# Optimization experiments

Measured on AMD Instinct MI355X. Metric: run time of the kernel, lower is better.

Reference implementation:

```python
import jax, jax.numpy as jnp
import numpy as np

NE = 50000   # num edges (nodes of the line graph)
NA = 800000  # adjacency pairs in the edge graph (~avg degree 16)
NC = 100000  # triadic candidates
F = 64       # edge_feat_dim
H = 128      # hidden_dim
L = 3        # num_layers


def setup_inputs() -> dict:
    key = jax.random.key(0)
    ks = iter(jax.random.split(key, 32))

    def w(shape, scale=0.05):
        return jax.random.normal(next(ks), shape, dtype=jnp.float32) * scale

    inp = {
        "edge_features": jax.random.normal(next(ks), (NE, F), dtype=jnp.float32),
        "adj_dst": jnp.sort(jax.random.randint(next(ks), (NA,), 0, NE)),
        "adj_src": jax.random.randint(next(ks), (NA,), 0, NE),
        "cand_i": jax.random.randint(next(ks), (NC,), 0, NE),
        "cand_j": jax.random.randint(next(ks), (NC,), 0, NE),
        # edge encoder: Linear(F,H) -> ReLU -> Linear(H,H)
        "enc_W1": w((F, H)), "enc_b1": jnp.zeros((H,), jnp.float32),
        "enc_W2": w((H, H)), "enc_b2": jnp.zeros((H,), jnp.float32),
        # per-layer message_net: Linear(2H,H) -> ReLU -> Linear(H,H)
        "msg_W1": w((L, 2 * H, H)), "msg_b1": jnp.zeros((L, H), jnp.float32),
        "msg_W2": w((L, H, H)), "msg_b2": jnp.zeros((L, H), jnp.float32),
        # per-layer update_net: Linear(2H,H) -> ReLU -> Linear(H,H)
        "upd_W1": w((L, 2 * H, H)), "upd_b1": jnp.zeros((L, H), jnp.float32),
        "upd_W2": w((L, H, H)), "upd_b2": jnp.zeros((L, H), jnp.float32),
        # triadic predictor: Linear(2H,H)->ReLU->Linear(H,H)->ReLU->Linear(H,1)
        "pred_W1": w((2 * H, H)), "pred_b1": jnp.zeros((H,), jnp.float32),
        "pred_W2": w((H, H)), "pred_b2": jnp.zeros((H,), jnp.float32),
        "pred_W3": w((H, 1)), "pred_b3": jnp.zeros((1,), jnp.float32),
    }
    return inp


def _mlp2(x, W1, b1, W2, b2):
    return jnp.maximum(x @ W1 + b1, 0.0) @ W2 + b2


def reference(edge_features, adj_dst, adj_src, cand_i, cand_j,
              enc_W1, enc_b1, enc_W2, enc_b2,
              msg_W1, msg_b1, msg_W2, msg_b2,
              upd_W1, upd_b1, upd_W2, upd_b2,
              pred_W1, pred_b1, pred_W2, pred_b2, pred_W3, pred_b3):
    # encode edge features -> [NE, H]
    e = _mlp2(edge_features, enc_W1, enc_b1, enc_W2, enc_b2)

    # degree of each edge-node in the line graph
    deg = jax.ops.segment_sum(jnp.ones((adj_dst.shape[0],), e.dtype), adj_dst,
                              num_segments=NE)  # [NE]
    inv_deg = 1.0 / jnp.maximum(deg, 1.0)
    isolated = (deg == 0.0)[:, None]

    for l in range(L):
        # per-pair message: message_net(concat(e_i, e_j))
        pair = jnp.concatenate([e[adj_dst], e[adj_src]], axis=-1)  # [NA, 2H]
        msgs = _mlp2(pair, msg_W1[l], msg_b1[l], msg_W2[l], msg_b2[l])  # [NA, H]
        agg = jax.ops.segment_sum(msgs, adj_dst, num_segments=NE) * inv_deg[:, None]
        # edges with no neighbors: message_net(concat(e_i, e_i))
        self_msg = _mlp2(jnp.concatenate([e, e], axis=-1),
                         msg_W1[l], msg_b1[l], msg_W2[l], msg_b2[l])
        message = jnp.where(isolated, self_msg, agg)
        # update: update_net(concat(e_i, message_i)), then outer ReLU
        e = _mlp2(jnp.concatenate([e, message], axis=-1),
                  upd_W1[l], upd_b1[l], upd_W2[l], upd_b2[l])
        e = jnp.maximum(e, 0.0)

    # triadic predictor on parent-edge pairs (dropout inactive at eval)
    comb = jnp.concatenate([e[cand_i], e[cand_j]], axis=-1)  # [NC, 2H]
    h = jnp.maximum(comb @ pred_W1 + pred_b1, 0.0)
    h = jnp.maximum(h @ pred_W2 + pred_b2, 0.0)
    logits = (h @ pred_W3 + pred_b3)[:, 0]  # [NC]
    probs = jax.nn.sigmoid(logits)
    return probs, logits
```

## Files before the change

### kernel.cpp

```cpp
#include <hip/hip_runtime.h>
#include <hip/hip_bf16.h>

#define NE 50000
#define NA 800000
#define NC 100000

typedef _Float16 f16;
typedef f16 half8 __attribute__((ext_vector_type(8)));
typedef f16 f16x2 __attribute__((ext_vector_type(2)));
typedef float f32x4 __attribute__((ext_vector_type(4)));

#define OFF_ENC1 0
#define OFF_ENC2 8192
#define OFF_MSGPQ 24576
#define OFF_UPD1 122880
#define OFF_UPD2 221184
#define OFF_PREDPQ 270336
#define OFF_PREDW2 303104
#define TOTAL_WT 319488

struct WTArgs {
    const float* src[20];
    int K[20];
    int dstOff[20];
    int dstStride[20];
    int cum[21];
};

__global__ void prep_kernel(WTArgs a, const float* __restrict__ x,
                            f16* __restrict__ wt, f16* __restrict__ xb,
                            int* __restrict__ degI) {
    int gid = blockIdx.x * 256 + threadIdx.x;
    if (gid < a.cum[20]) {
        int j = 0;
#pragma unroll
        for (int i = 1; i < 20; ++i) j += (gid >= a.cum[i]) ? 1 : 0;
        int e = gid - a.cum[j];
        int K = a.K[j];
        int k = e % K;
        int n = e / K;
        wt[a.dstOff[j] + n * a.dstStride[j] + k] = (f16)a.src[j][(size_t)k * 128 + n];
        return;
    }
    int g2 = gid - a.cum[20];
    if (g2 < NE * 16) {
        float4 v = ((const float4*)x)[g2];
        f16x2 p = {(f16)v.x, (f16)v.y}, q = {(f16)v.z, (f16)v.w};
        ((f16x2*)xb)[g2 * 2] = p;
        ((f16x2*)xb)[g2 * 2 + 1] = q;
        return;
    }
    int g3 = g2 - NE * 16;
    if (g3 < NE) degI[g3] = 0;
}

__global__ void fuse_w(const float* __restrict__ msg_W2, const float* __restrict__ msg_b2,
                       const float* __restrict__ upd_W1, const float* __restrict__ upd_b1,
                       f16* __restrict__ wt, float* __restrict__ fbias) {
    int gid = blockIdx.x * 256 + threadIdx.x;
    if (gid >= 3 * 128 * 129) return;
    int l = gid / (128 * 129);
    int rem = gid % (128 * 129);
    int n = rem / 129;
    int kk = rem % 129;
    const float* U1b = upd_W1 + (size_t)l * 32768 + 16384;
    if (kk < 128) {
        const float* w2row = msg_W2 + (size_t)l * 16384 + (size_t)kk * 128;
        float s = 0.0f;
        for (int m = 0; m < 128; ++m) s += w2row[m] * U1b[m * 128 + n];
        wt[OFF_UPD1 + l * 32768 + n * 256 + 128 + kk] = (f16)s;
    } else {
        const float* b2 = msg_b2 + l * 128;
        float s = upd_b1[l * 128 + n];
        for (int m = 0; m < 128; ++m) s += b2[m] * U1b[m * 128 + n];
        fbias[l * 128 + n] = s;
    }
}

__global__ void degseg_kernel(const int* __restrict__ adj_dst, int* __restrict__ degI,
                              int* __restrict__ segStart) {
    int i = blockIdx.x * 256 + threadIdx.x;
    if (i < NA) {
        int d = adj_dst[i];
        atomicAdd(&degI[d], 1);
        if (i == 0 || adj_dst[i - 1] != d) segStart[d] = i;
    }
}

__global__ __launch_bounds__(256) void pair_agg(
    const f16* __restrict__ P, const f16* __restrict__ Q,
    const int* __restrict__ adj_src, const int* __restrict__ segStart,
    const int* __restrict__ degI, f16* __restrict__ hbar) {
    int w = __builtin_amdgcn_readfirstlane(blockIdx.x * 4 + (threadIdx.x >> 6));
    if (w >= NE) return;
    int lane = threadIdx.x & 63;
    f16x2 p2 = ((const f16x2*)P)[(size_t)w * 64 + lane];
    float p0 = (float)p2.x, p1 = (float)p2.y;
    float a0, a1;
    int deg = degI[w];
    if (deg == 0) {
        f16x2 q2 = ((const f16x2*)Q)[(size_t)w * 64 + lane];
        a0 = fmaxf(p0 + (float)q2.x, 0.0f);
        a1 = fmaxf(p1 + (float)q2.y, 0.0f);
    } else {
        int s = segStart[w];
        float x0 = 0.0f, x1 = 0.0f, y0 = 0.0f, y1 = 0.0f;
        int j = 0;
        for (; j + 3 < deg; j += 4) {
            int s0 = adj_src[s + j], s1 = adj_src[s + j + 1];
            int s2 = adj_src[s + j + 2], s3 = adj_src[s + j + 3];
            f16x2 qa = ((const f16x2*)Q)[(size_t)s0 * 64 + lane];
            f16x2 qb = ((const f16x2*)Q)[(size_t)s1 * 64 + lane];
            f16x2 qc = ((const f16x2*)Q)[(size_t)s2 * 64 + lane];
            f16x2 qd = ((const f16x2*)Q)[(size_t)s3 * 64 + lane];
            x0 += fmaxf(p0 + (float)qa.x, 0.0f);
            x1 += fmaxf(p1 + (float)qa.y, 0.0f);
            y0 += fmaxf(p0 + (float)qb.x, 0.0f);
            y1 += fmaxf(p1 + (float)qb.y, 0.0f);
            x0 += fmaxf(p0 + (float)qc.x, 0.0f);
            x1 += fmaxf(p1 + (float)qc.y, 0.0f);
            y0 += fmaxf(p0 + (float)qd.x, 0.0f);
            y1 += fmaxf(p1 + (float)qd.y, 0.0f);
        }
        for (; j < deg; ++j) {
            int s0 = adj_src[s + j];
            f16x2 qa = ((const f16x2*)Q)[(size_t)s0 * 64 + lane];
            x0 += fmaxf(p0 + (float)qa.x, 0.0f);
            x1 += fmaxf(p1 + (float)qa.y, 0.0f);
        }
        float sc = 1.0f / (float)deg;
        a0 = (x0 + y0) * sc;
        a1 = (x1 + y1) * sc;
    }
    f16x2 o;
    o.x = (f16)a0;
    o.y = (f16)a1;
    ((f16x2*)hbar)[(size_t)w * 64 + lane] = o;
}

template <int K1, bool RELU_OUT>
__global__ __launch_bounds__(256, 2) void mlp2pq_kernel(
    const f16* __restrict__ in0, const f16* __restrict__ in1,
    const f16* __restrict__ w1t, const float* __restrict__ b1,
    const f16* __restrict__ w2t, const float* __restrict__ b2,
    f16* __restrict__ oute,
    const f16* __restrict__ wpq, const float* __restrict__ bP,
    f16* __restrict__ P, f16* __restrict__ Q, int numRows) {
    constexpr int KC1 = K1 / 32;
    constexpr int SA = K1 + 8;
    constexpr int SH = 136;
    constexpr int ABY = 64 * SA * 2;
    constexpr int HEBY = 64 * SH * 2 * 2;
    constexpr int BYTES = ABY > HEBY ? ABY : HEBY;
    __shared__ __align__(16) char U[BYTES];
    f16* Abuf = (f16*)U;
    f16* Hbuf = (f16*)U;
    f16* Ebuf = (f16*)(U + 64 * SH * 2);

    const int t = threadIdx.x;
    const int lane = t & 63, wave = t >> 6;
    const int quad = lane >> 4, mn = lane & 15;
    const int n0 = wave * 32;
    const int rbase = blockIdx.x << 6;

    constexpr int UPR = K1 / 8;
    constexpr int USH = (K1 == 256) ? 5 : 3;
#pragma unroll
    for (int it = 0; it < (64 * UPR) / 256; ++it) {
        int u = it * 256 + t;
        int row = u >> USH;
        int k = (u & (UPR - 1)) * 8;
        int gr = rbase + row;
        half8 v = {};
        if (gr < numRows) {
            const f16* src;
            if constexpr (K1 == 64)
                src = in0 + (size_t)gr * 64 + k;
            else
                src = (k < 128) ? (in0 + (size_t)gr * 128 + k)
                                : (in1 + (size_t)gr * 128 + (k - 128));
            v = *(const half8*)src;
        }
        *(half8*)(Abuf + row * SA + k) = v;
    }

    {
        half8 w1f[KC1][2];
#pragma unroll
        for (int kc = 0; kc < KC1; ++kc)
#pragma unroll
            for (int nt = 0; nt < 2; ++nt)
                w1f[kc][nt] = *(const half8*)(w1t + (size_t)(n0 + nt * 16 + mn) * K1 + kc * 32 + quad * 8);
        float b1c[2] = {b1[n0 + mn], b1[n0 + 16 + mn]};
        __syncthreads();

        f32x4 acc[4][2];
#pragma unroll
        for (int mt = 0; mt < 4; ++mt) {
            acc[mt][0] = (f32x4){b1c[0], b1c[0], b1c[0], b1c[0]};
            acc[mt][1] = (f32x4){b1c[1], b1c[1], b1c[1], b1c[1]};
        }
#pragma unroll
        for (int kc = 0; kc < KC1; ++kc) {
            half8 af[4];
#pragma unroll
            for (int mt = 0; mt < 4; ++mt)
                af[mt] = *(const half8*)(Abuf + (mt * 16 + mn) * SA + kc * 32 + quad * 8);
#pragma unroll
            for (int mt = 0; mt < 4; ++mt) {
                acc[mt][0] = __builtin_amdgcn_mfma_f32_16x16x32_f16(af[mt], w1f[kc][0], acc[mt][0], 0, 0, 0);
                acc[mt][1] = __builtin_amdgcn_mfma_f32_16x16x32_f16(af[mt], w1f[kc][1], acc[mt][1], 0, 0, 0);
            }
        }
        __syncthreads();
#pragma unroll
        for (int mt = 0; mt < 4; ++mt)
#pragma unroll
            for (int nt = 0; nt < 2; ++nt)
#pragma unroll
                for (int r = 0; r < 4; ++r)
                    Hbuf[(mt * 16 + quad * 4 + r) * SH + n0 + nt * 16 + mn] =
                        (f16)fmaxf(acc[mt][nt][r], 0.0f);
        __syncthreads();
    }

    {
        half8 w2f[4][2];
#pragma unroll
        for (int kc = 0; kc < 4; ++kc)
#pragma unroll
            for (int nt = 0; nt < 2; ++nt)
                w2f[kc][nt] = *(const half8*)(w2t + (size_t)(n0 + nt * 16 + mn) * 128 + kc * 32 + quad * 8);
        float b2c[2] = {b2[n0 + mn], b2[n0 + 16 + mn]};

        f32x4 acc2[4][2];
#pragma unroll
        for (int mt = 0; mt < 4; ++mt) {
            acc2[mt][0] = (f32x4){b2c[0], b2c[0], b2c[0], b2c[0]};
            acc2[mt][1] = (f32x4){b2c[1], b2c[1], b2c[1], b2c[1]};
        }
#pragma unroll
        for (int kc = 0; kc < 4; ++kc) {
            half8 af[4];
#pragma unroll
            for (int mt = 0; mt < 4; ++mt)
                af[mt] = *(const half8*)(Hbuf + (mt * 16 + mn) * SH + kc * 32 + quad * 8);
#pragma unroll
            for (int mt = 0; mt < 4; ++mt) {
                acc2[mt][0] = __builtin_amdgcn_mfma_f32_16x16x32_f16(af[mt], w2f[kc][0], acc2[mt][0], 0, 0, 0);
                acc2[mt][1] = __builtin_amdgcn_mfma_f32_16x16x32_f16(af[mt], w2f[kc][1], acc2[mt][1], 0, 0, 0);
            }
        }
#pragma unroll
        for (int mt = 0; mt < 4; ++mt)
#pragma unroll
            for (int nt = 0; nt < 2; ++nt)
#pragma unroll
                for (int r = 0; r < 4; ++r) {
                    float v = acc2[mt][nt][r];
                    if constexpr (RELU_OUT) v = fmaxf(v, 0.0f);
                    f16 hv = (f16)v;
                    int lr = mt * 16 + quad * 4 + r;
                    Ebuf[lr * SH + n0 + nt * 16 + mn] = hv;
                    int gr = rbase + lr;
                    if (gr < numRows) oute[(size_t)gr * 128 + n0 + nt * 16 + mn] = hv;
                }
        __syncthreads();
    }

    {
        half8 wpa[4][2];
#pragma unroll
        for (int kc = 0; kc < 4; ++kc)
#pragma unroll
            for (int nt = 0; nt < 2; ++nt)
                wpa[kc][nt] = *(const half8*)(wpq + (size_t)(n0 + nt * 16 + mn) * 128 + kc * 32 + quad * 8);
        float bpc[2] = {bP[n0 + mn], bP[n0 + 16 + mn]};
        f32x4 accp[4][2];
#pragma unroll
        for (int mt = 0; mt < 4; ++mt) {
            accp[mt][0] = (f32x4){bpc[0], bpc[0], bpc[0], bpc[0]};
            accp[mt][1] = (f32x4){bpc[1], bpc[1], bpc[1], bpc[1]};
        }
#pragma unroll
        for (int kc = 0; kc < 4; ++kc) {
            half8 af[4];
#pragma unroll
            for (int mt = 0; mt < 4; ++mt)
                af[mt] = *(const half8*)(Ebuf + (mt * 16 + mn) * SH + kc * 32 + quad * 8);
#pragma unroll
            for (int mt = 0; mt < 4; ++mt) {
                accp[mt][0] = __builtin_amdgcn_mfma_f32_16x16x32_f16(af[mt], wpa[kc][0], accp[mt][0], 0, 0, 0);
                accp[mt][1] = __builtin_amdgcn_mfma_f32_16x16x32_f16(af[mt], wpa[kc][1], accp[mt][1], 0, 0, 0);
            }
        }
#pragma unroll
        for (int mt = 0; mt < 4; ++mt)
#pragma unroll
            for (int nt = 0; nt < 2; ++nt)
#pragma unroll
                for (int r = 0; r < 4; ++r) {
                    int gr = rbase + mt * 16 + quad * 4 + r;
                    if (gr < numRows)
                        P[(size_t)gr * 128 + n0 + nt * 16 + mn] = (f16)accp[mt][nt][r];
                }
    }

    {
        half8 wpb[4][2];
#pragma unroll
        for (int kc = 0; kc < 4; ++kc)
#pragma unroll
            for (int nt = 0; nt < 2; ++nt)
                wpb[kc][nt] = *(const half8*)(wpq + 16384 + (size_t)(n0 + nt * 16 + mn) * 128 + kc * 32 + quad * 8);
        f32x4 accq[4][2];
#pragma unroll
        for (int mt = 0; mt < 4; ++mt) {
            accq[mt][0] = (f32x4){0.0f, 0.0f, 0.0f, 0.0f};
            accq[mt][1] = (f32x4){0.0f, 0.0f, 0.0f, 0.0f};
        }
#pragma unroll
        for (int kc = 0; kc < 4; ++kc) {
            half8 af[4];
#pragma unroll
            for (int mt = 0; mt < 4; ++mt)
                af[mt] = *(const half8*)(Ebuf + (mt * 16 + mn) * SH + kc * 32 + quad * 8);
#pragma unroll
            for (int mt = 0; mt < 4; ++mt) {
                accq[mt][0] = __builtin_amdgcn_mfma_f32_16x16x32_f16(af[mt], wpb[kc][0], accq[mt][0], 0, 0, 0);
                accq[mt][1] = __builtin_amdgcn_mfma_f32_16x16x32_f16(af[mt], wpb[kc][1], accq[mt][1], 0, 0, 0);
            }
        }
#pragma unroll
        for (int mt = 0; mt < 4; ++mt)
#pragma unroll
            for (int nt = 0; nt < 2; ++nt)
#pragma unroll
                for (int r = 0; r < 4; ++r) {
                    int gr = rbase + mt * 16 + quad * 4 + r;
                    if (gr < numRows)
                        Q[(size_t)gr * 128 + n0 + nt * 16 + mn] = (f16)accq[mt][nt][r];
                }
    }
}

__global__ __launch_bounds__(256, 2) void pred_tail(
    const f16* __restrict__ Pp, const f16* __restrict__ Qp,
    const int* __restrict__ ci, const int* __restrict__ cj,
    const f16* __restrict__ w2t, const float* __restrict__ b2,
    const float* __restrict__ w3, const float* __restrict__ b3,
    float* __restrict__ outProb, float* __restrict__ outLogit, int numRows) {
    constexpr int SA = 136;
    constexpr int SO = 133;
    constexpr int BYTES = (64 * SO * 4 > 64 * SA * 2) ? 64 * SO * 4 : 64 * SA * 2;
    __shared__ __align__(16) char U[BYTES];
    f16* Abuf = (f16*)U;
    float* Obuf = (float*)U;
    __shared__ float w3s[128];
    __shared__ float psum[256];

    const int t = threadIdx.x;
    const int lane = t & 63, wave = t >> 6;
    const int quad = lane >> 4, mn = lane & 15;
    const int n0 = wave * 32;

    if (t < 128) w3s[t] = w3[t];
    float b3v = b3[0];

    half8 wf[4][2];
#pragma unroll
    for (int kc = 0; kc < 4; ++kc)
#pragma unroll
        for (int nt = 0; nt < 2; ++nt)
            wf[kc][nt] = *(const half8*)(w2t + (size_t)(n0 + nt * 16 + mn) * 128 + kc * 32 + quad * 8);
    float b2c[2] = {b2[n0 + mn], b2[n0 + 16 + mn]};

    const int nTiles = (numRows + 63) >> 6;
    for (int tile = blockIdx.x; tile < nTiles; tile += gridDim.x) {
        const int rbase = tile << 6;
#pragma unroll
        for (int it = 0; it < 4; ++it) {
            int u = it * 256 + t;
            int row = u >> 4;
            int k = (u & 15) * 8;
            int gr = rbase + row;
            half8 v = {};
            if (gr < numRows) {
                int i = ci[gr], j = cj[gr];
                half8 a = *(const half8*)(Pp + (size_t)i * 128 + k);
                half8 b = *(const half8*)(Qp + (size_t)j * 128 + k);
#pragma unroll
                for (int x = 0; x < 8; ++x)
                    v[x] = (f16)fmaxf((float)a[x] + (float)b[x], 0.0f);
            }
            *(half8*)(Abuf + row * SA + k) = v;
        }
        __syncthreads();

        f32x4 acc[4][2];
#pragma unroll
        for (int mt = 0; mt < 4; ++mt) {
            acc[mt][0] = (f32x4){b2c[0], b2c[0], b2c[0], b2c[0]};
            acc[mt][1] = (f32x4){b2c[1], b2c[1], b2c[1], b2c[1]};
        }
#pragma unroll
        for (int kc = 0; kc < 4; ++kc) {
            half8 af[4];
#pragma unroll
            for (int mt = 0; mt < 4; ++mt)
                af[mt] = *(const half8*)(Abuf + (mt * 16 + mn) * SA + kc * 32 + quad * 8);
#pragma unroll
            for (int mt = 0; mt < 4; ++mt) {
                acc[mt][0] = __builtin_amdgcn_mfma_f32_16x16x32_f16(af[mt], wf[kc][0], acc[mt][0], 0, 0, 0);
                acc[mt][1] = __builtin_amdgcn_mfma_f32_16x16x32_f16(af[mt], wf[kc][1], acc[mt][1], 0, 0, 0);
            }
        }
        __syncthreads();
#pragma unroll
        for (int mt = 0; mt < 4; ++mt)
#pragma unroll
            for (int nt = 0; nt < 2; ++nt)
#pragma unroll
                for (int r = 0; r < 4; ++r)
                    Obuf[(mt * 16 + quad * 4 + r) * SO + n0 + nt * 16 + mn] =
                        fmaxf(acc[mt][nt][r], 0.0f);
        __syncthreads();
        {
            int row = t & 63, q4 = t >> 6;
            float s = 0.0f;
#pragma unroll
            for (int i = 0; i < 32; ++i)
                s += Obuf[row * SO + q4 * 32 + i] * w3s[q4 * 32 + i];
            psum[t] = s;
        }
        __syncthreads();
        if (t < 64) {
            int gr = rbase + t;
            if (gr < numRows) {
                float lg = psum[t] + psum[t + 64] + psum[t + 128] + psum[t + 192] + b3v;
                outLogit[gr] = lg;
                outProb[gr] = 1.0f / (1.0f + expf(-lg));
            }
        }
        __syncthreads();
    }
}

extern "C" void kernel_launch(void* const* d_in, const int* in_sizes, int n_in,
                              void* d_out, int out_size, void* d_ws, size_t ws_size,
                              hipStream_t stream) {
    const float* edge_features = (const float*)d_in[0];
    const int* adj_dst = (const int*)d_in[1];
    const int* adj_src = (const int*)d_in[2];
    const int* cand_i = (const int*)d_in[3];
    const int* cand_j = (const int*)d_in[4];
    const float* enc_W1 = (const float*)d_in[5];
    const float* enc_b1 = (const float*)d_in[6];
    const float* enc_W2 = (const float*)d_in[7];
    const float* enc_b2 = (const float*)d_in[8];
    const float* msg_W1 = (const float*)d_in[9];
    const float* msg_b1 = (const float*)d_in[10];
    const float* msg_W2 = (const float*)d_in[11];
    const float* msg_b2 = (const float*)d_in[12];
    const float* upd_W1 = (const float*)d_in[13];
    const float* upd_b1 = (const float*)d_in[14];
    const float* upd_W2 = (const float*)d_in[15];
    const float* upd_b2 = (const float*)d_in[16];
    const float* pred_W1 = (const float*)d_in[17];
    const float* pred_b1 = (const float*)d_in[18];
    const float* pred_W2 = (const float*)d_in[19];
    const float* pred_b2 = (const float*)d_in[20];
    const float* pred_W3 = (const float*)d_in[21];
    const float* pred_b3 = (const float*)d_in[22];

    char* ws = (char*)d_ws;
    size_t off = 0;
    auto alloc = [&](size_t bytes) -> void* {
        void* p = ws + off;
        off = (off + bytes + 255) & ~(size_t)255;
        return p;
    };
    f16* wt = (f16*)alloc((size_t)TOTAL_WT * 2);
    float* fbias = (float*)alloc(3 * 128 * 4);
    f16* xb = (f16*)alloc((size_t)NE * 64 * 2);
    f16* eA = (f16*)alloc((size_t)NE * 128 * 2);
    f16* eB = (f16*)alloc((size_t)NE * 128 * 2);
    f16* Pb = (f16*)alloc((size_t)NE * 128 * 2);
    f16* Qb = (f16*)alloc((size_t)NE * 128 * 2);
    f16* hbar = (f16*)alloc((size_t)NE * 128 * 2);
    int* degI = (int*)alloc((size_t)NE * 4);
    int* segStart = (int*)alloc((size_t)NE * 4);

    WTArgs wa;
    int idx = 0, c = 0;
    auto addj = [&](const float* s, int K, int o, int st) {
        wa.src[idx] = s; wa.K[idx] = K; wa.dstOff[idx] = o;
        wa.dstStride[idx] = st; wa.cum[idx] = c;
        c += K * 128; idx++;
    };
    addj(enc_W1, 64, OFF_ENC1, 64);
    addj(enc_W2, 128, OFF_ENC2, 128);
    for (int l = 0; l < 3; ++l) addj(msg_W1 + (size_t)l * 32768, 128, OFF_MSGPQ + l * 32768, 128);
    for (int l = 0; l < 3; ++l) addj(msg_W1 + (size_t)l * 32768 + 16384, 128, OFF_MSGPQ + l * 32768 + 16384, 128);
    for (int l = 0; l < 3; ++l) addj(upd_W1 + (size_t)l * 32768, 128, OFF_UPD1 + l * 32768, 256);
    for (int l = 0; l < 3; ++l) addj(upd_W2 + (size_t)l * 16384, 128, OFF_UPD2 + l * 16384, 128);
    addj(pred_W1, 128, OFF_PREDPQ, 128);
    addj(pred_W1 + 16384, 128, OFF_PREDPQ + 16384, 128);
    addj(pred_W2, 128, OFF_PREDW2, 128);
    for (int i = idx; i <= 20; ++i) wa.cum[i] = c;

    const int prepN = 270336 + NE * 16 + NE;
    prep_kernel<<<(prepN + 255) / 256, 256, 0, stream>>>(wa, edge_features, wt, xb, degI);
    fuse_w<<<(3 * 128 * 129 + 255) / 256, 256, 0, stream>>>(msg_W2, msg_b2, upd_W1, upd_b1, wt, fbias);
    degseg_kernel<<<(NA + 255) / 256, 256, 0, stream>>>(adj_dst, degI, segStart);

    const int tilesNE = (NE + 63) / 64;

    mlp2pq_kernel<64, false><<<tilesNE, 256, 0, stream>>>(
        xb, nullptr, wt + OFF_ENC1, enc_b1, wt + OFF_ENC2, enc_b2, eA,
        wt + OFF_MSGPQ, msg_b1, Pb, Qb, NE);

    f16* cur = eA;
    f16* nxt = eB;
    for (int l = 0; l < 3; ++l) {
        pair_agg<<<(NE + 3) / 4, 256, 0, stream>>>(Pb, Qb, adj_src, segStart, degI, hbar);
        const f16* wpq = (l < 2) ? (wt + OFF_MSGPQ + (l + 1) * 32768) : (wt + OFF_PREDPQ);
        const float* bP = (l < 2) ? (msg_b1 + (l + 1) * 128) : pred_b1;
        mlp2pq_kernel<256, true><<<tilesNE, 256, 0, stream>>>(
            cur, hbar, wt + OFF_UPD1 + l * 32768, fbias + l * 128,
            wt + OFF_UPD2 + l * 16384, upd_b2 + l * 128, nxt,
            wpq, bP, Pb, Qb, NE);
        f16* tmp = cur; cur = nxt; nxt = tmp;
    }

    float* outP = (float*)d_out;
    pred_tail<<<(NC + 63) / 64, 256, 0, stream>>>(
        Pb, Qb, cand_i, cand_j, wt + OFF_PREDW2, pred_b2, pred_W3, pred_b3,
        outP, outP + NC, NC);

    (void)in_sizes; (void)n_in; (void)out_size; (void)ws_size;
}
```

Before: 392.9 us.

## Fuse whole GNN into one cooperative persistent kernel with in-tile aggregation

Replaces the chain of separate kernels with a single cooperative kernel of 512 blocks that walks through prep, segment bounds, encoder, three update layers and the predictor, separated by grid syncs. Neighbour aggregation now happens inside the update tile and is written straight into shared memory, which removes the hbar buffer and the separate pair_agg launch. P/Q are double-buffered so layers do not overwrite inputs. Degree atomics are replaced by segment start/end markers, and weight fragments are loaded per k-chunk instead of all being held in registers. The risks are grid-sync overhead, lower occupancy for the gather-heavy aggregation done by only one wave per row, and a fallback multi-kernel path if the cooperative launch fails.

```diff
diff --git a/kernel.cpp b/kernel.cpp
--- a/kernel.cpp
+++ b/kernel.cpp
@@ -1,9 +1,12 @@
 #include <hip/hip_runtime.h>
+#include <hip/hip_cooperative_groups.h>
 #include <hip/hip_bf16.h>
 
 #define NE 50000
 #define NA 800000
 #define NC 100000
+
+namespace cg = cooperative_groups;
 
 typedef _Float16 f16;
 typedef f16 half8 __attribute__((ext_vector_type(8)));
@@ -19,524 +22,533 @@
 #define OFF_PREDW2 303104
 #define TOTAL_WT 319488
 
-struct WTArgs {
-    const float* src[20];
-    int K[20];
-    int dstOff[20];
-    int dstStride[20];
-    int cum[21];
+#define R_FUSE 49536
+#define R_WT 270336
+#define R_X 800000
+#define R_Z 50000
+#define PTOT (R_FUSE + R_WT + R_X + R_Z)
+
+struct KP {
+    const float* edge_features;
+    const int *adj_dst, *adj_src, *cand_i, *cand_j;
+    const float *enc_b1, *enc_b2;
+    const float *msg_b1, *msg_W2, *msg_b2;
+    const float *upd_W1, *upd_b1, *upd_b2;
+    const float *pred_b1, *pred_b2, *pred_W3, *pred_b3;
+    f16* wt;
+    float* fbias;
+    f16 *xb, *eA, *eB, *P0, *Q0, *P1, *Q1;
+    int *segStart, *segEnd;
+    float *outP, *outL;
+    const float* wsrc[20];
+    int wK[20], wOff[20], wStr[20], wCum[21];
 };
 
-__global__ void prep_kernel(WTArgs a, const float* __restrict__ x,
-                            f16* __restrict__ wt, f16* __restrict__ xb,
-                            int* __restrict__ degI) {
-    int gid = blockIdx.x * 256 + threadIdx.x;
-    if (gid < a.cum[20]) {
+
+__device__ __forceinline__ void prep_item(const KP& p, int gid) {
+    if (gid < R_FUSE) {
+        int g = gid >> 7, n = gid & 127;
+        int l = g / 129, kk = g % 129;
+        const float* U1b = p.upd_W1 + (size_t)l * 32768 + 16384;
+        if (kk < 128) {
+            const float* w2row = p.msg_W2 + (size_t)l * 16384 + (size_t)kk * 128;
+            float s = 0.f;
+            for (int m = 0; m < 128; ++m) s += w2row[m] * U1b[m * 128 + n];
+            p.wt[OFF_UPD1 + l * 32768 + n * 256 + 128 + kk] = (f16)s;
+        } else {
+            const float* b2 = p.msg_b2 + l * 128;
+            float s = p.upd_b1[l * 128 + n];
+            for (int m = 0; m < 128; ++m) s += b2[m] * U1b[m * 128 + n];
+            p.fbias[l * 128 + n] = s;
+        }
+    } else if (gid < R_FUSE + R_WT) {
+        int e = gid - R_FUSE;
         int j = 0;
 #pragma unroll
-        for (int i = 1; i < 20; ++i) j += (gid >= a.cum[i]) ? 1 : 0;
-        int e = gid - a.cum[j];
-        int K = a.K[j];
-        int k = e % K;
-        int n = e / K;
-        wt[a.dstOff[j] + n * a.dstStride[j] + k] = (f16)a.src[j][(size_t)k * 128 + n];
-        return;
-    }
-    int g2 = gid - a.cum[20];
-    if (g2 < NE * 16) {
-        float4 v = ((const float4*)x)[g2];
-        f16x2 p = {(f16)v.x, (f16)v.y}, q = {(f16)v.z, (f16)v.w};
-        ((f16x2*)xb)[g2 * 2] = p;
-        ((f16x2*)xb)[g2 * 2 + 1] = q;
-        return;
-    }
-    int g3 = g2 - NE * 16;
-    if (g3 < NE) degI[g3] = 0;
-}
-
-__global__ void fuse_w(const float* __restrict__ msg_W2, const float* __restrict__ msg_b2,
-                       const float* __restrict__ upd_W1, const float* __restrict__ upd_b1,
-                       f16* __restrict__ wt, float* __restrict__ fbias) {
-    int gid = blockIdx.x * 256 + threadIdx.x;
-    if (gid >= 3 * 128 * 129) return;
-    int l = gid / (128 * 129);
-    int rem = gid % (128 * 129);
-    int n = rem / 129;
-    int kk = rem % 129;
-    const float* U1b = upd_W1 + (size_t)l * 32768 + 16384;
-    if (kk < 128) {
-        const float* w2row = msg_W2 + (size_t)l * 16384 + (size_t)kk * 128;
-        float s = 0.0f;
-        for (int m = 0; m < 128; ++m) s += w2row[m] * U1b[m * 128 + n];
-        wt[OFF_UPD1 + l * 32768 + n * 256 + 128 + kk] = (f16)s;
-    } else {
-        const float* b2 = msg_b2 + l * 128;
-        float s = upd_b1[l * 128 + n];
-        for (int m = 0; m < 128; ++m) s += b2[m] * U1b[m * 128 + n];
-        fbias[l * 128 + n] = s;
-    }
-}
-
-__global__ void degseg_kernel(const int* __restrict__ adj_dst, int* __restrict__ degI,
-                              int* __restrict__ segStart) {
-    int i = blockIdx.x * 256 + threadIdx.x;
-    if (i < NA) {
-        int d = adj_dst[i];
-        atomicAdd(&degI[d], 1);
-        if (i == 0 || adj_dst[i - 1] != d) segStart[d] = i;
-    }
-}
-
-__global__ __launch_bounds__(256) void pair_agg(
-    const f16* __restrict__ P, const f16* __restrict__ Q,
+        for (int i = 1; i < 20; ++i) j += (e >= p.wCum[i]) ? 1 : 0;
+        int r = e - p.wCum[j];
+        int K = p.wK[j];
+        int k = r % K, n = r / K;
+        p.wt[p.wOff[j] + n * p.wStr[j] + k] = (f16)p.wsrc[j][(size_t)k * 128 + n];
+    } else if (gid < R_FUSE + R_WT + R_X) {
+        int g2 = gid - (R_FUSE + R_WT);
+        float4 v = ((const float4*)p.edge_features)[g2];
+        f16x2 a = {(f16)v.x, (f16)v.y}, b = {(f16)v.z, (f16)v.w};
+        ((f16x2*)p.xb)[g2 * 2] = a;
+        ((f16x2*)p.xb)[g2 * 2 + 1] = b;
+    } else if (gid < PTOT) {
+        int z = gid - (R_FUSE + R_WT + R_X);
+        p.segStart[z] = 0;
+        p.segEnd[z] = 0;
+    }
+}
+
+__device__ __forceinline__ void degseg_item(const KP& p, int i) {
+    int d = p.adj_dst[i];
+    if (i == 0 || p.adj_dst[i - 1] != d) p.segStart[d] = i;
+    if (i == NA - 1 || p.adj_dst[i + 1] != d) p.segEnd[d] = i + 1;
+}
+
+template <int K1, bool AGG>
+__device__ __forceinline__ void do_tile(
+    char* SMEM, int tile, const f16* __restrict__ in0,
+    const f16* __restrict__ Pin, const f16* __restrict__ Qin,
     const int* __restrict__ adj_src, const int* __restrict__ segStart,
-    const int* __restrict__ degI, f16* __restrict__ hbar) {
-    int w = __builtin_amdgcn_readfirstlane(blockIdx.x * 4 + (threadIdx.x >> 6));
-    if (w >= NE) return;
-    int lane = threadIdx.x & 63;
-    f16x2 p2 = ((const f16x2*)P)[(size_t)w * 64 + lane];
-    float p0 = (float)p2.x, p1 = (float)p2.y;
-    float a0, a1;
-    int deg = degI[w];
-    if (deg == 0) {
-        f16x2 q2 = ((const f16x2*)Q)[(size_t)w * 64 + lane];
-        a0 = fmaxf(p0 + (float)q2.x, 0.0f);
-        a1 = fmaxf(p1 + (float)q2.y, 0.0f);
-    } else {
-        int s = segStart[w];
-        float x0 = 0.0f, x1 = 0.0f, y0 = 0.0f, y1 = 0.0f;
-        int j = 0;
-        for (; j + 3 < deg; j += 4) {
-            int s0 = adj_src[s + j], s1 = adj_src[s + j + 1];
-            int s2 = adj_src[s + j + 2], s3 = adj_src[s + j + 3];
-            f16x2 qa = ((const f16x2*)Q)[(size_t)s0 * 64 + lane];
-            f16x2 qb = ((const f16x2*)Q)[(size_t)s1 * 64 + lane];
-            f16x2 qc = ((const f16x2*)Q)[(size_t)s2 * 64 + lane];
-            f16x2 qd = ((const f16x2*)Q)[(size_t)s3 * 64 + lane];
-            x0 += fmaxf(p0 + (float)qa.x, 0.0f);
-            x1 += fmaxf(p1 + (float)qa.y, 0.0f);
-            y0 += fmaxf(p0 + (float)qb.x, 0.0f);
-            y1 += fmaxf(p1 + (float)qb.y, 0.0f);
-            x0 += fmaxf(p0 + (float)qc.x, 0.0f);
-            x1 += fmaxf(p1 + (float)qc.y, 0.0f);
-            y0 += fmaxf(p0 + (float)qd.x, 0.0f);
-            y1 += fmaxf(p1 + (float)qd.y, 0.0f);
-        }
-        for (; j < deg; ++j) {
-            int s0 = adj_src[s + j];
-            f16x2 qa = ((const f16x2*)Q)[(size_t)s0 * 64 + lane];
-            x0 += fmaxf(p0 + (float)qa.x, 0.0f);
-            x1 += fmaxf(p1 + (float)qa.y, 0.0f);
-        }
-        float sc = 1.0f / (float)deg;
-        a0 = (x0 + y0) * sc;
-        a1 = (x1 + y1) * sc;
-    }
-    f16x2 o;
-    o.x = (f16)a0;
-    o.y = (f16)a1;
-    ((f16x2*)hbar)[(size_t)w * 64 + lane] = o;
-}
-
-template <int K1, bool RELU_OUT>
-__global__ __launch_bounds__(256, 2) void mlp2pq_kernel(
-    const f16* __restrict__ in0, const f16* __restrict__ in1,
-    const f16* __restrict__ w1t, const float* __restrict__ b1,
-    const f16* __restrict__ w2t, const float* __restrict__ b2,
+    const int* __restrict__ segEnd,
+    const f16* __restrict__ w1t, const int w1s, const float* __restrict__ b1v,
+    const f16* __restrict__ w2t, const float* __restrict__ b2v, const bool reluOut,
     f16* __restrict__ oute,
-    const f16* __restrict__ wpq, const float* __restrict__ bP,
-    f16* __restrict__ P, f16* __restrict__ Q, int numRows) {
-    constexpr int KC1 = K1 / 32;
+    const f16* __restrict__ wpq, const float* __restrict__ bPp,
+    f16* __restrict__ Pout, f16* __restrict__ Qout) {
     constexpr int SA = K1 + 8;
     constexpr int SH = 136;
-    constexpr int ABY = 64 * SA * 2;
-    constexpr int HEBY = 64 * SH * 2 * 2;
-    constexpr int BYTES = ABY > HEBY ? ABY : HEBY;
-    __shared__ __align__(16) char U[BYTES];
-    f16* Abuf = (f16*)U;
-    f16* Hbuf = (f16*)U;
-    f16* Ebuf = (f16*)(U + 64 * SH * 2);
-
-    const int t = threadIdx.x;
-    const int lane = t & 63, wave = t >> 6;
-    const int quad = lane >> 4, mn = lane & 15;
-    const int n0 = wave * 32;
-    const int rbase = blockIdx.x << 6;
-
-    constexpr int UPR = K1 / 8;
-    constexpr int USH = (K1 == 256) ? 5 : 3;
-#pragma unroll
-    for (int it = 0; it < (64 * UPR) / 256; ++it) {
-        int u = it * 256 + t;
-        int row = u >> USH;
-        int k = (u & (UPR - 1)) * 8;
-        int gr = rbase + row;
+    f16* Abuf = (f16*)SMEM;
+    f16* Hbuf = (f16*)SMEM;
+    f16* Ebuf = (f16*)(SMEM + 17408);
+    const int t = threadIdx.x, lane = t & 63, wave = t >> 6;
+    const int quad = lane >> 4, mn = lane & 15, n0 = wave * 32;
+    const int rbase = tile << 6;
+
+    if constexpr (K1 == 64) {
+#pragma unroll
+        for (int it = 0; it < 2; ++it) {
+            int u = it * 256 + t, row = u >> 3, k = (u & 7) * 8, gr = rbase + row;
+            half8 v = {};
+            if (gr < NE) v = *(const half8*)(in0 + (size_t)gr * 64 + k);
+            *(half8*)(Abuf + row * SA + k) = v;
+        }
+    } else {
+#pragma unroll
+        for (int it = 0; it < 4; ++it) {
+            int u = it * 256 + t, row = u >> 4, k = (u & 15) * 8, gr = rbase + row;
+            half8 v = {};
+            if (gr < NE) v = *(const half8*)(in0 + (size_t)gr * 128 + k);
+            *(half8*)(Abuf + row * SA + k) = v;
+        }
+    }
+    if constexpr (AGG) {
+        for (int i = 0; i < 16; ++i) {
+            int dst = rbase + wave * 16 + i;
+            float a0 = 0.f, a1 = 0.f;
+            if (dst < NE) {
+                f16x2 p2 = ((const f16x2*)Pin)[(size_t)dst * 64 + lane];
+                float pp0 = (float)p2.x, pp1 = (float)p2.y;
+                int s = segStart[dst];
+                int deg = segEnd[dst] - s;
+                if (deg == 0) {
+                    f16x2 q2 = ((const f16x2*)Qin)[(size_t)dst * 64 + lane];
+                    a0 = fmaxf(pp0 + (float)q2.x, 0.f);
+                    a1 = fmaxf(pp1 + (float)q2.y, 0.f);
+                } else {
+                    float x0 = 0.f, x1 = 0.f;
+                    int j = 0;
+                    for (; j + 7 < deg; j += 8) {
+                        f16x2 q[8];
+#pragma unroll
+                        for (int u2 = 0; u2 < 8; ++u2)
+                            q[u2] = ((const f16x2*)Qin)[(size_t)adj_src[s + j + u2] * 64 + lane];
+#pragma unroll
+                        for (int u2 = 0; u2 < 8; ++u2) {
+                            x0 += fmaxf(pp0 + (float)q[u2].x, 0.f);
+                            x1 += fmaxf(pp1 + (float)q[u2].y, 0.f);
+                        }
+                    }
+                    for (; j < deg; ++j) {
+                        f16x2 q2 = ((const f16x2*)Qin)[(size_t)adj_src[s + j] * 64 + lane];
+                        x0 += fmaxf(pp0 + (float)q2.x, 0.f);
+                        x1 += fmaxf(pp1 + (float)q2.y, 0.f);
+                    }
+                    float sc = 1.f / (float)deg;
+                    a0 = x0 * sc;
+                    a1 = x1 * sc;
+                }
+            }
+            f16x2 o = {(f16)a0, (f16)a1};
+            *(f16x2*)(Abuf + (wave * 16 + i) * SA + 128 + lane * 2) = o;
+        }
+    }
+    __syncthreads();
+
+    f32x4 acc[4][2];
+    {
+        float bb0 = b1v[n0 + mn], bb1 = b1v[n0 + 16 + mn];
+#pragma unroll
+        for (int mt = 0; mt < 4; ++mt) {
+            acc[mt][0] = (f32x4){bb0, bb0, bb0, bb0};
+            acc[mt][1] = (f32x4){bb1, bb1, bb1, bb1};
+        }
+    }
+#pragma unroll
+    for (int kc = 0; kc < K1 / 32; ++kc) {
+        half8 wA = *(const half8*)(w1t + (size_t)(n0 + mn) * w1s + kc * 32 + quad * 8);
+        half8 wB = *(const half8*)(w1t + (size_t)(n0 + 16 + mn) * w1s + kc * 32 + quad * 8);
+        half8 af[4];
+#pragma unroll
+        for (int mt = 0; mt < 4; ++mt)
+            af[mt] = *(const half8*)(Abuf + (mt * 16 + mn) * SA + kc * 32 + quad * 8);
+#pragma unroll
+        for (int mt = 0; mt < 4; ++mt) {
+            acc[mt][0] = __builtin_amdgcn_mfma_f32_16x16x32_f16(af[mt], wA, acc[mt][0], 0, 0, 0);
+            acc[mt][1] = __builtin_amdgcn_mfma_f32_16x16x32_f16(af[mt], wB, acc[mt][1], 0, 0, 0);
+        }
+    }
+    __syncthreads();
+#pragma unroll
+    for (int mt = 0; mt < 4; ++mt)
+#pragma unroll
+        for (int nt = 0; nt < 2; ++nt)
+#pragma unroll
+            for (int r = 0; r < 4; ++r)
+                Hbuf[(mt * 16 + quad * 4 + r) * SH + n0 + nt * 16 + mn] =
+                    (f16)fmaxf(acc[mt][nt][r], 0.f);
+    __syncthreads();
+
+    {
+        float bb0 = b2v[n0 + mn], bb1 = b2v[n0 + 16 + mn];
+#pragma unroll
+        for (int mt = 0; mt < 4; ++mt) {
+            acc[mt][0] = (f32x4){bb0, bb0, bb0, bb0};
+            acc[mt][1] = (f32x4){bb1, bb1, bb1, bb1};
+        }
+    }
+#pragma unroll
+    for (int kc = 0; kc < 4; ++kc) {
+        half8 wA = *(const half8*)(w2t + (size_t)(n0 + mn) * 128 + kc * 32 + quad * 8);
+        half8 wB = *(const half8*)(w2t + (size_t)(n0 + 16 + mn) * 128 + kc * 32 + quad * 8);
+        half8 af[4];
+#pragma unroll
+        for (int mt = 0; mt < 4; ++mt)
+            af[mt] = *(const half8*)(Hbuf + (mt * 16 + mn) * SH + kc * 32 + quad * 8);
+#pragma unroll
+        for (int mt = 0; mt < 4; ++mt) {
+            acc[mt][0] = __builtin_amdgcn_mfma_f32_16x16x32_f16(af[mt], wA, acc[mt][0], 0, 0, 0);
+            acc[mt][1] = __builtin_amdgcn_mfma_f32_16x16x32_f16(af[mt], wB, acc[mt][1], 0, 0, 0);
+        }
+    }
+#pragma unroll
+    for (int mt = 0; mt < 4; ++mt)
+#pragma unroll
+        for (int nt = 0; nt < 2; ++nt)
+#pragma unroll
+            for (int r = 0; r < 4; ++r) {
+                float v = acc[mt][nt][r];
+                if (reluOut) v = fmaxf(v, 0.f);
+                Ebuf[(mt * 16 + quad * 4 + r) * SH + n0 + nt * 16 + mn] = (f16)v;
+            }
+    __syncthreads();
+
+#pragma unroll
+    for (int it = 0; it < 4; ++it) {
+        int u = it * 256 + t, row = u >> 4, k = (u & 15) * 8, gr = rbase + row;
+        if (gr < NE) {
+            half8 v = *(const half8*)(Ebuf + row * SH + k);
+            *(half8*)(oute + (size_t)gr * 128 + k) = v;
+        }
+    }
+
+    {
+        float bb0 = bPp[n0 + mn], bb1 = bPp[n0 + 16 + mn];
+#pragma unroll
+        for (int mt = 0; mt < 4; ++mt) {
+            acc[mt][0] = (f32x4){bb0, bb0, bb0, bb0};
+            acc[mt][1] = (f32x4){bb1, bb1, bb1, bb1};
+        }
+    }
+#pragma unroll
+    for (int kc = 0; kc < 4; ++kc) {
+        half8 wA = *(const half8*)(wpq + (size_t)(n0 + mn) * 128 + kc * 32 + quad * 8);
+        half8 wB = *(const half8*)(wpq + (size_t)(n0 + 16 + mn) * 128 + kc * 32 + quad * 8);
+        half8 af[4];
+#pragma unroll
+        for (int mt = 0; mt < 4; ++mt)
+            af[mt] = *(const half8*)(Ebuf + (mt * 16 + mn) * SH + kc * 32 + quad * 8);
+#pragma unroll
+        for (int mt = 0; mt < 4; ++mt) {
+            acc[mt][0] = __builtin_amdgcn_mfma_f32_16x16x32_f16(af[mt], wA, acc[mt][0], 0, 0, 0);
+            acc[mt][1] = __builtin_amdgcn_mfma_f32_16x16x32_f16(af[mt], wB, acc[mt][1], 0, 0, 0);
+        }
+    }
+#pragma unroll
+    for (int mt = 0; mt < 4; ++mt)
+#pragma unroll
+        for (int nt = 0; nt < 2; ++nt)
+#pragma unroll
+            for (int r = 0; r < 4; ++r) {
+                int gr = rbase + mt * 16 + quad * 4 + r;
+                if (gr < NE)
+                    Pout[(size_t)gr * 128 + n0 + nt * 16 + mn] = (f16)acc[mt][nt][r];
+            }
+#pragma unroll
+    for (int mt = 0; mt < 4; ++mt) {
+        acc[mt][0] = (f32x4){0.f, 0.f, 0.f, 0.f};
+        acc[mt][1] = (f32x4){0.f, 0.f, 0.f, 0.f};
+    }
+#pragma unroll
+    for (int kc = 0; kc < 4; ++kc) {
+        half8 wA = *(const half8*)(wpq + 16384 + (size_t)(n0 + mn) * 128 + kc * 32 + quad * 8);
+        half8 wB = *(const half8*)(wpq + 16384 + (size_t)(n0 + 16 + mn) * 128 + kc * 32 + quad * 8);
+        half8 af[4];
+#pragma unroll
+        for (int mt = 0; mt < 4; ++mt)
+            af[mt] = *(const half8*)(Ebuf + (mt * 16 + mn) * SH + kc * 32 + quad * 8);
+#pragma unroll
+        for (int mt = 0; mt < 4; ++mt) {
+            acc[mt][0] = __builtin_amdgcn_mfma_f32_16x16x32_f16(af[mt], wA, acc[mt][0], 0, 0, 0);
+            acc[mt][1] = __builtin_amdgcn_mfma_f32_16x16x32_f16(af[mt], wB, acc[mt][1], 0, 0, 0);
+        }
+    }
+#pragma unroll
+    for (int mt = 0; mt < 4; ++mt)
+#pragma unroll
+        for (int nt = 0; nt < 2; ++nt)
+#pragma unroll
+            for (int r = 0; r < 4; ++r) {
+                int gr = rbase + mt * 16 + quad * 4 + r;
+                if (gr < NE)
+                    Qout[(size_t)gr * 128 + n0 + nt * 16 + mn] = (f16)acc[mt][nt][r];
+            }
+    __syncthreads();
+}
+
+__device__ __forceinline__ void pred_tile(const KP& p, char* SMEM, float* w3s,
+                                          float* psum, int tile, float b3v) {
+    constexpr int SA = 136, SO = 133;
+    f16* Abuf = (f16*)SMEM;
+    float* Obuf = (float*)SMEM;
+    const int t = threadIdx.x, lane = t & 63, wave = t >> 6;
+    const int quad = lane >> 4, mn = lane & 15, n0 = wave * 32;
+    const int rbase = tile << 6;
+#pragma unroll
+    for (int it = 0; it < 4; ++it) {
+        int u = it * 256 + t, row = u >> 4, k = (u & 15) * 8, gr = rbase + row;
         half8 v = {};
-        if (gr < numRows) {
-            const f16* src;
-            if constexpr (K1 == 64)
-                src = in0 + (size_t)gr * 64 + k;
-            else
-                src = (k < 128) ? (in0 + (size_t)gr * 128 + k)
-                                : (in1 + (size_t)gr * 128 + (k - 128));
-            v = *(const half8*)src;
+        if (gr < NC) {
+            int ii = p.cand_i[gr], jj = p.cand_j[gr];
+            half8 a = *(const half8*)(p.P1 + (size_t)ii * 128 + k);
+            half8 b = *(const half8*)(p.Q1 + (size_t)jj * 128 + k);
+#pragma unroll
+            for (int x = 0; x < 8; ++x)
+                v[x] = (f16)fmaxf((float)a[x] + (float)b[x], 0.f);
         }
         *(half8*)(Abuf + row * SA + k) = v;
     }
-
+    __syncthreads();
+    f32x4 acc[4][2];
     {
-        half8 w1f[KC1][2];
-#pragma unroll
-        for (int kc = 0; kc < KC1; ++kc)
-#pragma unroll
-            for (int nt = 0; nt < 2; ++nt)
-                w1f[kc][nt] = *(const half8*)(w1t + (size_t)(n0 + nt * 16 + mn) * K1 + kc * 32 + quad * 8);
-        float b1c[2] = {b1[n0 + mn], b1[n0 + 16 + mn]};
-        __syncthreads();
-
-        f32x4 acc[4][2];
-#pragma unroll
-        for (int mt = 0; mt < 4; ++mt) {
-            acc[mt][0] = (f32x4){b1c[0], b1c[0], b1c[0], b1c[0]};
-            acc[mt][1] = (f32x4){b1c[1], b1c[1], b1c[1], b1c[1]};
-        }
-#pragma unroll
-        for (int kc = 0; kc < KC1; ++kc) {
-            half8 af[4];
-#pragma unroll
-            for (int mt = 0; mt < 4; ++mt)
-                af[mt] = *(const half8*)(Abuf + (mt * 16 + mn) * SA + kc * 32 + quad * 8);
-#pragma unroll
-            for (int mt = 0; mt < 4; ++mt) {
-                acc[mt][0] = __builtin_amdgcn_mfma_f32_16x16x32_f16(af[mt], w1f[kc][0], acc[mt][0], 0, 0, 0);
-                acc[mt][1] = __builtin_amdgcn_mfma_f32_16x16x32_f16(af[mt], w1f[kc][1], acc[mt][1], 0, 0, 0);
-            }
-        }
-        __syncthreads();
+        float bb0 = p.pred_b2[n0 + mn], bb1 = p.pred_b2[n0 + 16 + mn];
+#pragma unroll
+        for (int mt = 0; mt < 4; ++mt) {
+            acc[mt][0] = (f32x4){bb0, bb0, bb0, bb0};
+            acc[mt][1] = (f32x4){bb1, bb1, bb1, bb1};
+        }
+    }
+#pragma unroll
+    for (int kc = 0; kc < 4; ++kc) {
+        half8 wA = *(const half8*)(p.wt + OFF_PREDW2 + (size_t)(n0 + mn) * 128 + kc * 32 + quad * 8);
+        half8 wB = *(const half8*)(p.wt + OFF_PREDW2 + (size_t)(n0 + 16 + mn) * 128 + kc * 32 + quad * 8);
+        half8 af[4];
 #pragma unroll
         for (int mt = 0; mt < 4; ++mt)
-#pragma unroll
-            for (int nt = 0; nt < 2; ++nt)
-#pragma unroll
-                for (int r = 0; r < 4; ++r)
-                    Hbuf[(mt * 16 + quad * 4 + r) * SH + n0 + nt * 16 + mn] =
-                        (f16)fmaxf(acc[mt][nt][r], 0.0f);
-        __syncthreads();
-    }
-
+            af[mt] = *(const half8*)(Abuf + (mt * 16 + mn) * SA + kc * 32 + quad * 8);
+#pragma unroll
+        for (int mt = 0; mt < 4; ++mt) {
+            acc[mt][0] = __builtin_amdgcn_mfma_f32_16x16x32_f16(af[mt], wA, acc[mt][0], 0, 0, 0);
+            acc[mt][1] = __builtin_amdgcn_mfma_f32_16x16x32_f16(af[mt], wB, acc[mt][1], 0, 0, 0);
+        }
+    }
+    __syncthreads();
+#pragma unroll
+    for (int mt = 0; mt < 4; ++mt)
+#pragma unroll
+        for (int nt = 0; nt < 2; ++nt)
+#pragma unroll
+            for (int r = 0; r < 4; ++r)
+                Obuf[(mt * 16 + quad * 4 + r) * SO + n0 + nt * 16 + mn] =
+                    fmaxf(acc[mt][nt][r], 0.f);
+    __syncthreads();
     {
-        half8 w2f[4][2];
-#pragma unroll
-        for (int kc = 0; kc < 4; ++kc)
-#pragma unroll
-            for (int nt = 0; nt < 2; ++nt)
-                w2f[kc][nt] = *(const half8*)(w2t + (size_t)(n0 + nt * 16 + mn) * 128 + kc * 32 + quad * 8);
-        float b2c[2] = {b2[n0 + mn], b2[n0 + 16 + mn]};
-
-        f32x4 acc2[4][2];
-#pragma unroll
-        for (int mt = 0; mt < 4; ++mt) {
-            acc2[mt][0] = (f32x4){b2c[0], b2c[0], b2c[0], b2c[0]};
-            acc2[mt][1] = (f32x4){b2c[1], b2c[1], b2c[1], b2c[1]};
-        }
-#pragma unroll
-        for (int kc = 0; kc < 4; ++kc) {
-            half8 af[4];
-#pragma unroll
-            for (int mt = 0; mt < 4; ++mt)
-                af[mt] = *(const half8*)(Hbuf + (mt * 16 + mn) * SH + kc * 32 + quad * 8);
-#pragma unroll
-            for (int mt = 0; mt < 4; ++mt) {
-                acc2[mt][0] = __builtin_amdgcn_mfma_f32_16x16x32_f16(af[mt], w2f[kc][0], acc2[mt][0], 0, 0, 0);
-                acc2[mt][1] = __builtin_amdgcn_mfma_f32_16x16x32_f16(af[mt], w2f[kc][1], acc2[mt][1], 0, 0, 0);
-            }
-        }
-#pragma unroll
-        for (int mt = 0; mt < 4; ++mt)
-#pragma unroll
-            for (int nt = 0; nt < 2; ++nt)
-#pragma unroll
-                for (int r = 0; r < 4; ++r) {
-                    float v = acc2[mt][nt][r];
-                    if constexpr (RELU_OUT) v = fmaxf(v, 0.0f);
-                    f16 hv = (f16)v;
-                    int lr = mt * 16 + quad * 4 + r;
-                    Ebuf[lr * SH + n0 + nt * 16 + mn] = hv;
-                    int gr = rbase + lr;
-                    if (gr < numRows) oute[(size_t)gr * 128 + n0 + nt * 16 + mn] = hv;
-                }
-        __syncthreads();
-    }
-
-    {
-        half8 wpa[4][2];
-#pragma unroll
-        for (int kc = 0; kc < 4; ++kc)
-#pragma unroll
-            for (int nt = 0; nt < 2; ++nt)
-                wpa[kc][nt] = *(const half8*)(wpq + (size_t)(n0 + nt * 16 + mn) * 128 + kc * 32 + quad * 8);
-        float bpc[2] = {bP[n0 + mn], bP[n0 + 16 + mn]};
-        f32x4 accp[4][2];
-#pragma unroll
-        for (int mt = 0; mt < 4; ++mt) {
-            accp[mt][0] = (f32x4){bpc[0], bpc[0], bpc[0], bpc[0]};
-            accp[mt][1] = (f32x4){bpc[1], bpc[1], bpc[1], bpc[1]};
-        }
-#pragma unroll
-        for (int kc = 0; kc < 4; ++kc) {
-            half8 af[4];
-#pragma unroll
-            for (int mt = 0; mt < 4; ++mt)
-                af[mt] = *(const half8*)(Ebuf + (mt * 16 + mn) * SH + kc * 32 + quad * 8);
-#pragma unroll
-            for (int mt = 0; mt < 4; ++mt) {
-                accp[mt][0] = __builtin_amdgcn_mfma_f32_16x16x32_f16(af[mt], wpa[kc][0], accp[mt][0], 0, 0, 0);
-                accp[mt][1] = __builtin_amdgcn_mfma_f32_16x16x32_f16(af[mt], wpa[kc][1], accp[mt][1], 0, 0, 0);
-            }
-        }
-#pragma unroll
-        for (int mt = 0; mt < 4; ++mt)
-#pragma unroll
-            for (int nt = 0; nt < 2; ++nt)
-#pragma unroll
-                for (int r = 0; r < 4; ++r) {
-                    int gr = rbase + mt * 16 + quad * 4 + r;
-                    if (gr < numRows)
-                        P[(size_t)gr * 128 + n0 + nt * 16 + mn] = (f16)accp[mt][nt][r];
-                }
-    }
-
-    {
-        half8 wpb[4][2];
-#pragma unroll
-        for (int kc = 0; kc < 4; ++kc)
-#pragma unroll
-            for (int nt = 0; nt < 2; ++nt)
-                wpb[kc][nt] = *(const half8*)(wpq + 16384 + (size_t)(n0 + nt * 16 + mn) * 128 + kc * 32 + quad * 8);
-        f32x4 accq[4][2];
-#pragma unroll
-        for (int mt = 0; mt < 4; ++mt) {
-            accq[mt][0] = (f32x4){0.0f, 0.0f, 0.0f, 0.0f};
-            accq[mt][1] = (f32x4){0.0f, 0.0f, 0.0f, 0.0f};
-        }
-#pragma unroll
-        for (int kc = 0; kc < 4; ++kc) {
-            half8 af[4];
-#pragma unroll
-            for (int mt = 0; mt < 4; ++mt)
-                af[mt] = *(const half8*)(Ebuf + (mt * 16 + mn) * SH + kc * 32 + quad * 8);
-#pragma unroll
-            for (int mt = 0; mt < 4; ++mt) {
-                accq[mt][0] = __builtin_amdgcn_mfma_f32_16x16x32_f16(af[mt], wpb[kc][0], accq[mt][0], 0, 0, 0);
-                accq[mt][1] = __builtin_amdgcn_mfma_f32_16x16x32_f16(af[mt], wpb[kc][1], accq[mt][1], 0, 0, 0);
-            }
-        }
-#pragma unroll
-        for (int mt = 0; mt < 4; ++mt)
-#pragma unroll
-            for (int nt = 0; nt < 2; ++nt)
-#pragma unroll
-                for (int r = 0; r < 4; ++r) {
-                    int gr = rbase + mt * 16 + quad * 4 + r;
-                    if (gr < numRows)
-                        Q[(size_t)gr * 128 + n0 + nt * 16 + mn] = (f16)accq[mt][nt][r];
-                }
-    }
-}
-
-__global__ __launch_bounds__(256, 2) void pred_tail(
-    const f16* __restrict__ Pp, const f16* __restrict__ Qp,
-    const int* __restrict__ ci, const int* __restrict__ cj,
-    const f16* __restrict__ w2t, const float* __restrict__ b2,
-    const float* __restrict__ w3, const float* __restrict__ b3,
-    float* __restrict__ outProb, float* __restrict__ outLogit, int numRows) {
-    constexpr int SA = 136;
-    constexpr int SO = 133;
-    constexpr int BYTES = (64 * SO * 4 > 64 * SA * 2) ? 64 * SO * 4 : 64 * SA * 2;
-    __shared__ __align__(16) char U[BYTES];
-    f16* Abuf = (f16*)U;
-    float* Obuf = (float*)U;
+        int row = t & 63, q4 = t >> 6;
+        float s = 0.f;
+#pragma unroll
+        for (int i = 0; i < 32; ++i)
+            s += Obuf[row * SO + q4 * 32 + i] * w3s[q4 * 32 + i];
+        psum[t] = s;
+    }
+    __syncthreads();
+    if (t < 64) {
+        int gr = rbase + t;
+        if (gr < NC) {
+            float lg = psum[t] + psum[t + 64] + psum[t + 128] + psum[t + 192] + b3v;
+            p.outL[gr] = lg;
+            p.outP[gr] = 1.f / (1.f + expf(-lg));
+        }
+    }
+    __syncthreads();
+}
+
+__device__ __forceinline__ void upd_layer_ptrs(const KP& p, int l,
+    const f16*& ein, f16*& eout, const f16*& Pin, const f16*& Qin,
+    f16*& Pout, f16*& Qout, const f16*& wpq, const float*& bP) {
+    ein = (l & 1) ? p.eB : p.eA;
+    eout = (l & 1) ? p.eA : p.eB;
+    Pin = (l & 1) ? p.P1 : p.P0;
+    Qin = (l & 1) ? p.Q1 : p.Q0;
+    Pout = (l & 1) ? p.P0 : p.P1;
+    Qout = (l & 1) ? p.Q0 : p.Q1;
+    wpq = (l < 2) ? (p.wt + OFF_MSGPQ + (l + 1) * 32768) : (p.wt + OFF_PREDPQ);
+    bP = (l < 2) ? (p.msg_b1 + (l + 1) * 128) : p.pred_b1;
+}
+
+__global__ __launch_bounds__(256, 2) void gnn_all(KP p) {
+    cg::grid_group gg = cg::this_grid();
+    __shared__ __align__(16) char SMEM[34816];
     __shared__ float w3s[128];
     __shared__ float psum[256];
-
     const int t = threadIdx.x;
-    const int lane = t & 63, wave = t >> 6;
-    const int quad = lane >> 4, mn = lane & 15;
-    const int n0 = wave * 32;
-
-    if (t < 128) w3s[t] = w3[t];
-    float b3v = b3[0];
-
-    half8 wf[4][2];
-#pragma unroll
-    for (int kc = 0; kc < 4; ++kc)
-#pragma unroll
-        for (int nt = 0; nt < 2; ++nt)
-            wf[kc][nt] = *(const half8*)(w2t + (size_t)(n0 + nt * 16 + mn) * 128 + kc * 32 + quad * 8);
-    float b2c[2] = {b2[n0 + mn], b2[n0 + 16 + mn]};
-
-    const int nTiles = (numRows + 63) >> 6;
-    for (int tile = blockIdx.x; tile < nTiles; tile += gridDim.x) {
-        const int rbase = tile << 6;
-#pragma unroll
-        for (int it = 0; it < 4; ++it) {
-            int u = it * 256 + t;
-            int row = u >> 4;
-            int k = (u & 15) * 8;
-            int gr = rbase + row;
-            half8 v = {};
-            if (gr < numRows) {
-                int i = ci[gr], j = cj[gr];
-                half8 a = *(const half8*)(Pp + (size_t)i * 128 + k);
-                half8 b = *(const half8*)(Qp + (size_t)j * 128 + k);
-#pragma unroll
-                for (int x = 0; x < 8; ++x)
-                    v[x] = (f16)fmaxf((float)a[x] + (float)b[x], 0.0f);
-            }
-            *(half8*)(Abuf + row * SA + k) = v;
-        }
-        __syncthreads();
-
-        f32x4 acc[4][2];
-#pragma unroll
-        for (int mt = 0; mt < 4; ++mt) {
-            acc[mt][0] = (f32x4){b2c[0], b2c[0], b2c[0], b2c[0]};
-            acc[mt][1] = (f32x4){b2c[1], b2c[1], b2c[1], b2c[1]};
-        }
-#pragma unroll
-        for (int kc = 0; kc < 4; ++kc) {
-            half8 af[4];
-#pragma unroll
-            for (int mt = 0; mt < 4; ++mt)
-                af[mt] = *(const half8*)(Abuf + (mt * 16 + mn) * SA + kc * 32 + quad * 8);
-#pragma unroll
-            for (int mt = 0; mt < 4; ++mt) {
-                acc[mt][0] = __builtin_amdgcn_mfma_f32_16x16x32_f16(af[mt], wf[kc][0], acc[mt][0], 0, 0, 0);
-                acc[mt][1] = __builtin_amdgcn_mfma_f32_16x16x32_f16(af[mt], wf[kc][1], acc[mt][1], 0, 0, 0);
-            }
-        }
-        __syncthreads();
-#pragma unroll
-        for (int mt = 0; mt < 4; ++mt)
-#pragma unroll
-            for (int nt = 0; nt < 2; ++nt)
-#pragma unroll
-                for (int r = 0; r < 4; ++r)
-                    Obuf[(mt * 16 + quad * 4 + r) * SO + n0 + nt * 16 + mn] =
-                        fmaxf(acc[mt][nt][r], 0.0f);
-        __syncthreads();
-        {
-            int row = t & 63, q4 = t >> 6;
-            float s = 0.0f;
-#pragma unroll
-            for (int i = 0; i < 32; ++i)
-                s += Obuf[row * SO + q4 * 32 + i] * w3s[q4 * 32 + i];
-            psum[t] = s;
-        }
-        __syncthreads();
-        if (t < 64) {
-            int gr = rbase + t;
-            if (gr < numRows) {
-                float lg = psum[t] + psum[t + 64] + psum[t + 128] + psum[t + 192] + b3v;
-                outLogit[gr] = lg;
-                outProb[gr] = 1.0f / (1.0f + expf(-lg));
-            }
-        }
-        __syncthreads();
-    }
+    const int gsz = gridDim.x * 256;
+    const int g0 = blockIdx.x * 256 + t;
+
+    for (int gid = g0; gid < PTOT; gid += gsz) prep_item(p, gid);
+    gg.sync();
+
+    for (int tile = blockIdx.x; tile < (NE + 63) / 64; tile += gridDim.x)
+        do_tile<64, false>(SMEM, tile, p.xb, nullptr, nullptr, nullptr, nullptr, nullptr,
+                           p.wt + OFF_ENC1, 64, p.enc_b1, p.wt + OFF_ENC2, p.enc_b2, false,
+                           p.eA, p.wt + OFF_MSGPQ, p.msg_b1, p.P0, p.Q0);
+    for (int i = g0; i < NA; i += gsz) degseg_item(p, i);
+
+    for (int l = 0; l < 3; ++l) {
+        gg.sync();
+        const f16 *ein, *Pin, *Qin, *wpq;
+        f16 *eout, *Pout, *Qout;
+        const float* bP;
+        upd_layer_ptrs(p, l, ein, eout, Pin, Qin, Pout, Qout, wpq, bP);
+        for (int tile = blockIdx.x; tile < (NE + 63) / 64; tile += gridDim.x)
+            do_tile<256, true>(SMEM, tile, ein, Pin, Qin, p.adj_src, p.segStart, p.segEnd,
+                               p.wt + OFF_UPD1 + l * 32768, 256, p.fbias + l * 128,
+                               p.wt + OFF_UPD2 + l * 16384, p.upd_b2 + l * 128, true,
+                               eout, wpq, bP, Pout, Qout);
+    }
+    gg.sync();
+
+    if (t < 128) w3s[t] = p.pred_W3[t];
+    float b3v = p.pred_b3[0];
+    for (int tile = blockIdx.x; tile < (NC + 63) / 64; tile += gridDim.x)
+        pred_tile(p, SMEM, w3s, psum, tile, b3v);
+}
+
+__global__ void k_prep(KP p) {
+    int gid = blockIdx.x * 256 + threadIdx.x;
+    if (gid < PTOT) prep_item(p, gid);
+}
+__global__ void k_degseg(KP p) {
+    int i = blockIdx.x * 256 + threadIdx.x;
+    if (i < NA) degseg_item(p, i);
+}
+__global__ __launch_bounds__(256, 2) void k_enc(KP p) {
+    __shared__ __align__(16) char SMEM[34816];
+    do_tile<64, false>(SMEM, blockIdx.x, p.xb, nullptr, nullptr, nullptr, nullptr, nullptr,
+                       p.wt + OFF_ENC1, 64, p.enc_b1, p.wt + OFF_ENC2, p.enc_b2, false,
+                       p.eA, p.wt + OFF_MSGPQ, p.msg_b1, p.P0, p.Q0);
+}
+__global__ __launch_bounds__(256, 2) void k_upd(KP p, int l) {
+    __shared__ __align__(16) char SMEM[34816];
+    const f16 *ein, *Pin, *Qin, *wpq;
+    f16 *eout, *Pout, *Qout;
+    const float* bP;
+    upd_layer_ptrs(p, l, ein, eout, Pin, Qin, Pout, Qout, wpq, bP);
+    do_tile<256, true>(SMEM, blockIdx.x, ein, Pin, Qin, p.adj_src, p.segStart, p.segEnd,
+                       p.wt + OFF_UPD1 + l * 32768, 256, p.fbias + l * 128,
+                       p.wt + OFF_UPD2 + l * 16384, p.upd_b2 + l * 128, true,
+                       eout, wpq, bP, Pout, Qout);
+}
+__global__ __launch_bounds__(256, 2) void k_pred(KP p) {
+    __shared__ __align__(16) char SMEM[34816];
+    __shared__ float w3s[128];
+    __shared__ float psum[256];
+    if (threadIdx.x < 128) w3s[threadIdx.x] = p.pred_W3[threadIdx.x];
+    float b3v = p.pred_b3[0];
+    pred_tile(p, SMEM, w3s, psum, blockIdx.x, b3v);
 }
 
 extern "C" void kernel_launch(void* const* d_in, const int* in_sizes, int n_in,
                               void* d_out, int out_size, void* d_ws, size_t ws_size,
                               hipStream_t stream) {
-    const float* edge_features = (const float*)d_in[0];
-    const int* adj_dst = (const int*)d_in[1];
-    const int* adj_src = (const int*)d_in[2];
-    const int* cand_i = (const int*)d_in[3];
-    const int* cand_j = (const int*)d_in[4];
+    KP p;
+    p.edge_features = (const float*)d_in[0];
+    p.adj_dst = (const int*)d_in[1];
+    p.adj_src = (const int*)d_in[2];
+    p.cand_i = (const int*)d_in[3];
+    p.cand_j = (const int*)d_in[4];
     const float* enc_W1 = (const float*)d_in[5];
-    const float* enc_b1 = (const float*)d_in[6];
+    p.enc_b1 = (const float*)d_in[6];
     const float* enc_W2 = (const float*)d_in[7];
-    const float* enc_b2 = (const float*)d_in[8];
+    p.enc_b2 = (const float*)d_in[8];
     const float* msg_W1 = (const float*)d_in[9];
-    const float* msg_b1 = (const float*)d_in[10];
-    const float* msg_W2 = (const float*)d_in[11];
-    const float* msg_b2 = (const float*)d_in[12];
-    const float* upd_W1 = (const float*)d_in[13];
-    const float* upd_b1 = (const float*)d_in[14];
+    p.msg_b1 = (const float*)d_in[10];
+    p.msg_W2 = (const float*)d_in[11];
+    p.msg_b2 = (const float*)d_in[12];
+    p.upd_W1 = (const float*)d_in[13];
+    p.upd_b1 = (const float*)d_in[14];
     const float* upd_W2 = (const float*)d_in[15];
-    const float* upd_b2 = (const float*)d_in[16];
+    p.upd_b2 = (const float*)d_in[16];
     const float* pred_W1 = (const float*)d_in[17];
-    const float* pred_b1 = (const float*)d_in[18];
+    p.pred_b1 = (const float*)d_in[18];
     const float* pred_W2 = (const float*)d_in[19];
-    const float* pred_b2 = (const float*)d_in[20];
-    const float* pred_W3 = (const float*)d_in[21];
-    const float* pred_b3 = (const float*)d_in[22];
+    p.pred_b2 = (const float*)d_in[20];
+    p.pred_W3 = (const float*)d_in[21];
+    p.pred_b3 = (const float*)d_in[22];
 
     char* ws = (char*)d_ws;
     size_t off = 0;
     auto alloc = [&](size_t bytes) -> void* {
-        void* p = ws + off;
+        void* q = ws + off;
         off = (off + bytes + 255) & ~(size_t)255;
-        return p;
+        return q;
     };
-    f16* wt = (f16*)alloc((size_t)TOTAL_WT * 2);
-    float* fbias = (float*)alloc(3 * 128 * 4);
-    f16* xb = (f16*)alloc((size_t)NE * 64 * 2);
-    f16* eA = (f16*)alloc((size_t)NE * 128 * 2);
-    f16* eB = (f16*)alloc((size_t)NE * 128 * 2);
-    f16* Pb = (f16*)alloc((size_t)NE * 128 * 2);
-    f16* Qb = (f16*)alloc((size_t)NE * 128 * 2);
-    f16* hbar = (f16*)alloc((size_t)NE * 128 * 2);
-    int* degI = (int*)alloc((size_t)NE * 4);
-    int* segStart = (int*)alloc((size_t)NE * 4);
-
-    WTArgs wa;
+    p.wt = (f16*)alloc((size_t)TOTAL_WT * 2);
+    p.fbias = (float*)alloc(3 * 128 * 4);
+    p.xb = (f16*)alloc((size_t)NE * 64 * 2);
+    p.eA = (f16*)alloc((size_t)NE * 128 * 2);
+    p.eB = (f16*)alloc((size_t)NE * 128 * 2);
+    p.P0 = (f16*)alloc((size_t)NE * 128 * 2);
+    p.Q0 = (f16*)alloc((size_t)NE * 128 * 2);
+    p.P1 = (f16*)alloc((size_t)NE * 128 * 2);
+    p.Q1 = (f16*)alloc((size_t)NE * 128 * 2);
+    p.segStart = (int*)alloc((size_t)NE * 4);
+    p.segEnd = (int*)alloc((size_t)NE * 4);
+    p.outP = (float*)d_out;
+    p.outL = (float*)d_out + NC;
+
     int idx = 0, c = 0;
     auto addj = [&](const float* s, int K, int o, int st) {
-        wa.src[idx] = s; wa.K[idx] = K; wa.dstOff[idx] = o;
-        wa.dstStride[idx] = st; wa.cum[idx] = c;
+        p.wsrc[idx] = s; p.wK[idx] = K; p.wOff[idx] = o;
+        p.wStr[idx] = st; p.wCum[idx] = c;
         c += K * 128; idx++;
     };
     addj(enc_W1, 64, OFF_ENC1, 64);
     addj(enc_W2, 128, OFF_ENC2, 128);
     for (int l = 0; l < 3; ++l) addj(msg_W1 + (size_t)l * 32768, 128, OFF_MSGPQ + l * 32768, 128);
     for (int l = 0; l < 3; ++l) addj(msg_W1 + (size_t)l * 32768 + 16384, 128, OFF_MSGPQ + l * 32768 + 16384, 128);
-    for (int l = 0; l < 3; ++l) addj(upd_W1 + (size_t)l * 32768, 128, OFF_UPD1 + l * 32768, 256);
+    for (int l = 0; l < 3; ++l) addj(p.upd_W1 + (size_t)l * 32768, 128, OFF_UPD1 + l * 32768, 256);
     for (int l = 0; l < 3; ++l) addj(upd_W2 + (size_t)l * 16384, 128, OFF_UPD2 + l * 16384, 128);
     addj(pred_W1, 128, OFF_PREDPQ, 128);
     addj(pred_W1 + 16384, 128, OFF_PREDPQ + 16384, 128);
     addj(pred_W2, 128, OFF_PREDW2, 128);
-    for (int i = idx; i <= 20; ++i) wa.cum[i] = c;
-
-    const int prepN = 270336 + NE * 16 + NE;
-    prep_kernel<<<(prepN + 255) / 256, 256, 0, stream>>>(wa, edge_features, wt, xb, degI);
-    fuse_w<<<(3 * 128 * 129 + 255) / 256, 256, 0, stream>>>(msg_W2, msg_b2, upd_W1, upd_b1, wt, fbias);
-    degseg_kernel<<<(NA + 255) / 256, 256, 0, stream>>>(adj_dst, degI, segStart);
-
-    const int tilesNE = (NE + 63) / 64;
-
-    mlp2pq_kernel<64, false><<<tilesNE, 256, 0, stream>>>(
-        xb, nullptr, wt + OFF_ENC1, enc_b1, wt + OFF_ENC2, enc_b2, eA,
-        wt + OFF_MSGPQ, msg_b1, Pb, Qb, NE);
-
-    f16* cur = eA;
-    f16* nxt = eB;
-    for (int l = 0; l < 3; ++l) {
-        pair_agg<<<(NE + 3) / 4, 256, 0, stream>>>(Pb, Qb, adj_src, segStart, degI, hbar);
-        const f16* wpq = (l < 2) ? (wt + OFF_MSGPQ + (l + 1) * 32768) : (wt + OFF_PREDPQ);
-        const float* bP = (l < 2) ? (msg_b1 + (l + 1) * 128) : pred_b1;
-        mlp2pq_kernel<256, true><<<tilesNE, 256, 0, stream>>>(
-            cur, hbar, wt + OFF_UPD1 + l * 32768, fbias + l * 128,
-            wt + OFF_UPD2 + l * 16384, upd_b2 + l * 128, nxt,
-            wpq, bP, Pb, Qb, NE);
-        f16* tmp = cur; cur = nxt; nxt = tmp;
-    }
-
-    float* outP = (float*)d_out;
-    pred_tail<<<(NC + 63) / 64, 256, 0, stream>>>(
-        Pb, Qb, cand_i, cand_j, wt + OFF_PREDW2, pred_b2, pred_W3, pred_b3,
-        outP, outP + NC, NC);
+    for (int i = idx; i <= 20; ++i) p.wCum[i] = c;
+
+    void* args[] = {(void*)&p};
+    hipError_t le = hipLaunchCooperativeKernel(gnn_all, dim3(512), dim3(256), args, 0, stream);
+    if (le != hipSuccess) {
+        (void)hipGetLastError();
+        const int tilesNE = (NE + 63) / 64;
+        const int tilesNC = (NC + 63) / 64;
+        k_prep<<<(PTOT + 255) / 256, 256, 0, stream>>>(p);
+        k_degseg<<<(NA + 255) / 256, 256, 0, stream>>>(p);
+        k_enc<<<tilesNE, 256, 0, stream>>>(p);
+        for (int l = 0; l < 3; ++l) k_upd<<<tilesNE, 256, 0, stream>>>(p, l);
+        k_pred<<<tilesNC, 256, 0, stream>>>(p);
+    }
 
     (void)in_sizes; (void)n_in; (void)out_size; (void)ws_size;
 }
```

After: 930.6 us. 137% more time.
